# Performance work log

Hardware: AMD Instinct MI355X
Metric: run time of the kernel (lower is better)

The kernel has to match this reference:

```python
import jax, jax.numpy as jnp
import numpy as np

N, D, H, E = 50000, 128, 128, 800000

def _layernorm(h, g, b, eps=1e-5):
    m = jnp.mean(h, axis=-1, keepdims=True)
    v = jnp.mean((h - m) ** 2, axis=-1, keepdims=True)
    return (h - m) * jax.lax.rsqrt(v + eps) * g + b

def setup_inputs() -> dict:
    key = jax.random.key(0)
    ks = jax.random.split(key, 24)
    s = 0.02
    inp = {
        "x": jax.random.normal(ks[0], (N, D), dtype=jnp.float32),
        "edge_index": jax.random.randint(ks[1], (2, E), 0, N, dtype=jnp.int64),
        "degree": jax.random.uniform(ks[2], (N, 1), dtype=jnp.float32) * 32.0,
        "W_lin": jax.random.normal(ks[3], (D, H), jnp.float32) * s,
        "b_lin": jnp.zeros((H,), jnp.float32),
        "Wa1": jax.random.normal(ks[4], (H, H), jnp.float32) * s,
        "ba1": jnp.zeros((H,), jnp.float32),
        "Wa2": jax.random.normal(ks[5], (H, H), jnp.float32) * s,
        "ba2": jnp.zeros((H,), jnp.float32),
        "Wb1": jax.random.normal(ks[6], (H, H), jnp.float32) * s,
        "bb1": jnp.zeros((H,), jnp.float32),
        "Wb2": jax.random.normal(ks[7], (H, H), jnp.float32) * s,
        "bb2": jnp.zeros((H,), jnp.float32),
        "Wg1": jax.random.normal(ks[8], (H, H), jnp.float32) * s,
        "bg1": jnp.zeros((H,), jnp.float32),
        "Wg2": jax.random.normal(ks[9], (H, H), jnp.float32) * s,
        "bg2": jnp.zeros((H,), jnp.float32),
        "Wf1": jax.random.normal(ks[10], (H, H), jnp.float32) * s,
        "bf1": jnp.zeros((H,), jnp.float32),
        "Wf2": jax.random.normal(ks[11], (H, H), jnp.float32) * s,
        "bf2": jnp.zeros((H,), jnp.float32),
        "ln_g": jnp.ones((H,), jnp.float32),
        "ln_b": jnp.zeros((H,), jnp.float32),
    }
    return inp

def reference(x, edge_index, degree, W_lin, b_lin, Wa1, ba1, Wa2, ba2,
              Wb1, bb1, Wb2, bb2, Wg1, bg1, Wg2, bg2, Wf1, bf1, Wf2, bf2,
              ln_g, ln_b):
    # Dropout layers are identity (eval mode)
    h = x @ W_lin + b_lin                                  # [N,H]
    x_res = _layernorm(h, ln_g, ln_b)
    alpha = jax.nn.softplus(jax.nn.relu(h @ Wa1 + ba1) @ Wa2 + ba2)
    beta = jax.nn.softplus(jax.nn.relu(h @ Wb1 + bb1) @ Wb2 + bb2)
    gamma = jax.nn.gelu(h @ Wg1 + bg1, approximate=False) @ Wg2 + bg2
    src, dst = edge_index[0], edge_index[1]
    agg = jax.ops.segment_sum(h[src], dst, num_segments=h.shape[0])  # [N,H]
    y = (beta * agg + gamma) / (alpha + beta * degree)
    z = jax.nn.gelu(y @ Wf1 + bf1, approximate=False) @ Wf2 + bf2
    return z + x_res
```

## Files before the change

kernel.cpp:

```cpp
#include <hip/hip_runtime.h>
#include <hip/hip_bf16.h>
#include <math.h>

#define NODES 50000
#define NEDGE 800000
#define NT_TILES 782
#define NBUCK 98
#define BSHIFT 9
#define BCAP 10240
#define NP1 195
#define EPB1 4104

typedef __bf16 bf16_t;
typedef __bf16 bf16x8 __attribute__((ext_vector_type(8)));
typedef float floatx4 __attribute__((ext_vector_type(4)));

__device__ __forceinline__ float bfbits2f(unsigned int hi16) {
    union { unsigned int u; float f; } c; c.u = hi16; return c.f;
}
__device__ __forceinline__ unsigned short f2bfbits(float f) {
    bf16_t b = (bf16_t)f; unsigned short u;
    __builtin_memcpy(&u, &b, 2); return u;
}

__device__ __forceinline__ float act_rt(float v, int act) {
    if (act == 1) return fmaxf(v, 0.f);
    if (act == 2) {
        float w = 0.79788456f * (v + 0.044715f * v * v * v);
        float e = __expf(2.f * w);
        float th = 1.f - 2.f / (e + 1.f);
        return 0.5f * v * (1.f + th);
    }
    if (act == 3) return fmaxf(v, 0.f) + __logf(1.f + __expf(-fabsf(v)));
    return v;
}

__global__ __launch_bounds__(256) void prep_w_zero(
    const float* __restrict__ w0, const float* __restrict__ w1,
    const float* __restrict__ w2, const float* __restrict__ w3,
    const float* __restrict__ w4, const float* __restrict__ w5,
    const float* __restrict__ w6, const float* __restrict__ w7,
    const float* __restrict__ w8, bf16_t* __restrict__ wt,
    int* __restrict__ gcur)
{
    if (blockIdx.x >= 9) {
        if (threadIdx.x < NBUCK) gcur[threadIdx.x] = 0;
        return;
    }
    const float* Ws[9] = {w0, w1, w2, w3, w4, w5, w6, w7, w8};
    const float* W = Ws[blockIdx.x];
    bf16_t* o = wt + blockIdx.x * 16384;
    for (int idx = threadIdx.x; idx < 16384; idx += 256) {
        int k = idx >> 7, n = idx & 127;
        o[n * 128 + k] = (bf16_t)W[idx];
    }
}

__device__ __forceinline__ void load_w_regs(const bf16_t* __restrict__ W,
                                            uint4 (&wr)[8], int t)
{
    for (int i = 0; i < 8; ++i) {
        int c = t + i * 256;
        int row = c >> 4, g = c & 15;
        wr[i] = *(const uint4*)(W + row * 128 + g * 8);
    }
}
__device__ __forceinline__ void store_w_regs(const uint4 (&wr)[8],
                                             bf16_t* Bs, int t)
{
    for (int i = 0; i < 8; ++i) {
        int c = t + i * 256;
        int row = c >> 4, g = c & 15;
        *(uint4*)&Bs[row * 128 + ((g ^ (row & 15)) * 8)] = wr[i];
    }
}
__device__ __forceinline__ void afrag_gbf16(const bf16_t* __restrict__ A,
        bf16x8 (&af)[4], int r0, int lane, int wave, int M)
{
    int gr = r0 + wave * 16 + (lane & 15);
    gr = min(gr, M - 1);
    const bf16_t* p = A + (size_t)gr * 128 + (lane >> 4) * 8;
    for (int kc = 0; kc < 4; ++kc)
        af[kc] = *(const bf16x8*)(p + kc * 32);
}
__device__ __forceinline__ void kloop64(const bf16x8 (&af)[4], const bf16_t* Bs,
                                        floatx4 (&acc)[8], int l15, int quad)
{
    for (int ni = 0; ni < 8; ++ni)
        for (int r = 0; r < 4; ++r) acc[ni][r] = 0.f;
    for (int kc = 0; kc < 4; ++kc) {
        int kg = kc * 4 + quad;
        bf16x8 b[8];
        for (int ni = 0; ni < 8; ++ni) {
            int row = ni * 16 + l15;
            b[ni] = *(const bf16x8*)&Bs[row * 128 + ((kg ^ l15) * 8)];
        }
        for (int ni = 0; ni < 8; ++ni)
            acc[ni] = __builtin_amdgcn_mfma_f32_16x16x32_bf16(
                af[kc], b[ni], acc[ni], 0, 0, 0);
    }
}
__device__ __forceinline__ void write_Csw(bf16_t* Csw, floatx4 (&acc)[8],
        const float (&bias_r)[8], int lane, int wave, int act)
{
    const int l15 = lane & 15, quad = lane >> 4;
    for (int ni = 0; ni < 8; ++ni) {
        int col = ni * 16 + l15;
        for (int r = 0; r < 4; ++r) {
            int row = wave * 16 + quad * 4 + r;
            float v = act_rt(acc[ni][r] + bias_r[ni], act);
            Csw[row * 128 + (((col >> 3) ^ (row & 15)) << 3) + (col & 7)] = (bf16_t)v;
        }
    }
}
__device__ __forceinline__ void afrag_Csw(const bf16_t* Csw, bf16x8 (&af)[4],
                                          int lane, int wave)
{
    int l15 = lane & 15, quad = lane >> 4;
    int row = wave * 16 + l15;
    for (int kc = 0; kc < 4; ++kc) {
        int kg = kc * 4 + quad;
        af[kc] = *(const bf16x8*)&Csw[row * 128 + ((kg ^ l15) * 8)];
    }
}
__device__ __forceinline__ void copy_Csw_out(const bf16_t* Csw,
        bf16_t* __restrict__ out, int t, int r0, int M)
{
    for (int i = 0; i < 4; ++i) {
        int c = t + i * 256;
        int row = c >> 4, g = c & 15;
        int gr = r0 + row;
        if (gr < M)
            *(uint4*)(out + (size_t)gr * 128 + g * 8) =
                *(const uint4*)&Csw[row * 128 + ((g ^ (row & 15)) * 8)];
    }
}

__global__ __launch_bounds__(256, 3) void hln_p1(
    const float* __restrict__ x, const bf16_t* __restrict__ wt,
    const float* __restrict__ b_lin,
    const float* __restrict__ ln_g, const float* __restrict__ ln_b,
    bf16_t* __restrict__ h, bf16_t* __restrict__ xres,
    const int* __restrict__ ei, int* __restrict__ gcur,
    unsigned* __restrict__ ebuf, int M)
{
    __shared__ __align__(16) char smem[49152];
    const int t = threadIdx.x;
    const int bid = blockIdx.x;

    if (bid % 5 == 4) {
        int* lcnt  = (int*)smem;
        int* lbase = lcnt + NBUCK;
        if (t < NBUCK) lcnt[t] = 0;
        __syncthreads();
        int p1id = bid / 5;
        int base = p1id * EPB1;
        int e_end = min(base + EPB1, NEDGE);
        for (int e = base + t; e < e_end; e += 256)
            atomicAdd(&lcnt[ei[NEDGE + e] >> BSHIFT], 1);
        __syncthreads();
        if (t < NBUCK) {
            lbase[t] = atomicAdd(&gcur[t], lcnt[t]);
            lcnt[t] = 0;
        }
        __syncthreads();
        for (int e = base + t; e < e_end; e += 256) {
            int d = ei[NEDGE + e];
            int s = ei[e];
            int b = d >> BSHIFT;
            int off = atomicAdd(&lcnt[b], 1);
            int pos = lbase[b] + off;
            if (pos < BCAP)
                ebuf[(size_t)b * BCAP + pos] =
                    (unsigned)s | ((unsigned)(d & 511) << 16);
        }
        return;
    }

    bf16_t* Bs  = (bf16_t*)smem;
    bf16_t* Csw = (bf16_t*)(smem + 32768);
    const int tile = bid - bid / 5;
    const int r0 = tile * 64;
    const int lane = t & 63, wave = t >> 6, l15 = lane & 15, quad = lane >> 4;
    uint4 wr[8];
    bf16x8 af[4];
    floatx4 acc[8];
    float bias_r[8];
    for (int ni = 0; ni < 8; ++ni) bias_r[ni] = b_lin[ni * 16 + l15];

    {
        int gr = min(r0 + wave * 16 + l15, M - 1);
        const float* p = x + (size_t)gr * 128 + quad * 8;
        for (int kc = 0; kc < 4; ++kc) {
            float4 u0 = *(const float4*)(p + kc * 32);
            float4 u1 = *(const float4*)(p + kc * 32 + 4);
            bf16x8 f;
            f[0] = (bf16_t)u0.x; f[1] = (bf16_t)u0.y;
            f[2] = (bf16_t)u0.z; f[3] = (bf16_t)u0.w;
            f[4] = (bf16_t)u1.x; f[5] = (bf16_t)u1.y;
            f[6] = (bf16_t)u1.z; f[7] = (bf16_t)u1.w;
            af[kc] = f;
        }
    }
    load_w_regs(wt, wr, t);
    store_w_regs(wr, Bs, t);
    __syncthreads();
    kloop64(af, Bs, acc, l15, quad);
    write_Csw(Csw, acc, bias_r, lane, wave, 0);
    __syncthreads();

    int row = t >> 2, p4 = t & 3;
    int gr = r0 + row;
    uint4 raw[4];
    float vals[32];
    float s = 0.f, sq = 0.f;
    for (int i = 0; i < 4; ++i) {
        int lg = p4 * 4 + i;
        raw[i] = *(const uint4*)&Csw[row * 128 + ((lg ^ (row & 15)) * 8)];
        const unsigned* u = (const unsigned*)&raw[i];
        for (int k = 0; k < 4; ++k) {
            float f0 = bfbits2f(u[k] << 16);
            float f1 = bfbits2f(u[k] & 0xffff0000u);
            vals[i * 8 + k * 2] = f0; vals[i * 8 + k * 2 + 1] = f1;
            s += f0 + f1; sq += f0 * f0 + f1 * f1;
        }
    }
    s += __shfl_xor(s, 1, 64);  sq += __shfl_xor(sq, 1, 64);
    s += __shfl_xor(s, 2, 64);  sq += __shfl_xor(sq, 2, 64);
    float m   = s * (1.f / 128.f);
    float var = fmaxf(sq * (1.f / 128.f) - m * m, 0.f);
    float rs  = rsqrtf(var + 1e-5f);
    if (gr < M) {
        for (int i = 0; i < 4; ++i) {
            int lg = p4 * 4 + i;
            *(uint4*)(h + (size_t)gr * 128 + lg * 8) = raw[i];
            unsigned short ob[8];
            for (int k = 0; k < 8; ++k) {
                int col = lg * 8 + k;
                ob[k] = f2bfbits((vals[i * 8 + k] - m) * rs * ln_g[col] + ln_b[col]);
            }
            uint4 o;
            o.x = ob[0] | ((unsigned)ob[1] << 16);
            o.y = ob[2] | ((unsigned)ob[3] << 16);
            o.z = ob[4] | ((unsigned)ob[5] << 16);
            o.w = ob[6] | ((unsigned)ob[7] << 16);
            *(uint4*)(xres + (size_t)gr * 128 + lg * 8) = o;
        }
    }
}

__global__ __launch_bounds__(256, 3) void branch_p2(
    const bf16_t* __restrict__ h, const bf16_t* __restrict__ wt,
    const float* __restrict__ ba1, const float* __restrict__ ba2,
    const float* __restrict__ bb1, const float* __restrict__ bb2,
    const float* __restrict__ bg1, const float* __restrict__ bg2,
    bf16_t* __restrict__ al, bf16_t* __restrict__ be, bf16_t* __restrict__ ga,
    const int* __restrict__ gcur, const unsigned* __restrict__ ebuf,
    int* __restrict__ off_start, int* __restrict__ cntN,
    int* __restrict__ srcs, int M)
{
    __shared__ __align__(16) char smem[49152];
    const int t = threadIdx.x;
    const int bid = blockIdx.x;

    if (bid % 25 == 24) {
        int* ncnt = (int*)smem;
        int* sa   = ncnt + 512;
        int* sb   = sa + 512;
        int* ncur = sb + 512;
        int* red  = ncur + 512;
        const int b = bid / 25;
        int total = min(gcur[b], BCAP);

        int v = 0;
        for (int j = t; j < b; j += 256) v += min(gcur[j], BCAP);
        for (int o = 1; o < 64; o <<= 1) v += __shfl_xor(v, o, 64);
        if ((t & 63) == 0) red[t >> 6] = v;
        ncnt[t] = 0; ncnt[t + 256] = 0;
        __syncthreads();
        int bucketBase = red[0] + red[1] + red[2] + red[3];

        const unsigned* eb = ebuf + (size_t)b * BCAP;
        for (int i = t; i < total; i += 256)
            atomicAdd(&ncnt[eb[i] >> 16], 1);
        __syncthreads();
        sa[t] = ncnt[t]; sa[t + 256] = ncnt[t + 256];
        __syncthreads();
        int* pin = sa; int* pout = sb;
        for (int o = 1; o < 512; o <<= 1) {
            for (int j = t; j < 512; j += 256)
                pout[j] = pin[j] + (j >= o ? pin[j - o] : 0);
            __syncthreads();
            int* tmp = pin; pin = pout; pout = tmp;
        }
        for (int j = t; j < 512; j += 256) {
            int excl = pin[j] - ncnt[j];
            int node = (b << BSHIFT) + j;
            if (node < NODES) {
                off_start[node] = bucketBase + excl;
                cntN[node] = ncnt[j];
            }
            ncur[j] = excl;
        }
        __syncthreads();
        for (int i = t; i < total; i += 256) {
            unsigned p = eb[i];
            int dl = p >> 16;
            int pos = atomicAdd(&ncur[dl], 1);
            srcs[bucketBase + pos] = (int)(p & 0xFFFFu);
        }
        return;
    }

    const int tile = bid - bid / 25;
    if (tile >= 3 * NT_TILES) return;
    bf16_t* Bs  = (bf16_t*)smem;
    bf16_t* Csw = (bf16_t*)(smem + 32768);
    const int branch = tile / NT_TILES;
    const int r0 = (tile % NT_TILES) * 64;
    const int lane = t & 63, wave = t >> 6, l15 = lane & 15, quad = lane >> 4;
    uint4 wr[8];
    bf16x8 af[4];
    floatx4 acc[8];

    const bf16_t* w1 = wt + (1 + 2 * branch) * 16384;
    const bf16_t* w2 = wt + (2 + 2 * branch) * 16384;
    const float* b1p = (branch == 0) ? ba1 : (branch == 1) ? bb1 : bg1;
    const float* b2p = (branch == 0) ? ba2 : (branch == 1) ? bb2 : bg2;
    bf16_t* out = (branch == 0) ? al : (branch == 1) ? be : ga;
    const int act1 = (branch == 2) ? 2 : 1;
    const int act2 = (branch == 2) ? 0 : 3;

    float b1_r[8], b2_r[8];
    for (int ni = 0; ni < 8; ++ni) {
        b1_r[ni] = b1p[ni * 16 + l15];
        b2_r[ni] = b2p[ni * 16 + l15];
    }

    afrag_gbf16(h, af, r0, lane, wave, M);
    load_w_regs(w1, wr, t);
    store_w_regs(wr, Bs, t);
    load_w_regs(w2, wr, t);
    __syncthreads();

    kloop64(af, Bs, acc, l15, quad);
    write_Csw(Csw, acc, b1_r, lane, wave, act1);
    __syncthreads();
    store_w_regs(wr, Bs, t);
    __syncthreads();

    afrag_Csw(Csw, af, lane, wave);
    kloop64(af, Bs, acc, l15, quad);
    __syncthreads();
    write_Csw(Csw, acc, b2_r, lane, wave, act2);
    __syncthreads();
    copy_Csw_out(Csw, out, t, r0, M);
}

__global__ __launch_bounds__(256, 3) void fused_out(
    const bf16_t* __restrict__ y, const bf16_t* __restrict__ wt,
    const float* __restrict__ bf1, const float* __restrict__ bf2,
    const bf16_t* __restrict__ xres, float* __restrict__ out, int M)
{
    __shared__ __align__(16) char smem[49152];
    bf16_t* Bs  = (bf16_t*)smem;
    bf16_t* Csw = (bf16_t*)(smem + 32768);
    float*  Cf  = (float*)smem;
    const int t = threadIdx.x;
    const int r0 = blockIdx.x * 64;
    const int lane = t & 63, wave = t >> 6, l15 = lane & 15, quad = lane >> 4;
    uint4 wr[8];
    bf16x8 af[4];
    floatx4 acc[8];

    float b1_r[8], b2_r[8];
    for (int ni = 0; ni < 8; ++ni) {
        b1_r[ni] = bf1[ni * 16 + l15];
        b2_r[ni] = bf2[ni * 16 + l15];
    }

    afrag_gbf16(y, af, r0, lane, wave, M);
    load_w_regs(wt + 7 * 16384, wr, t);
    store_w_regs(wr, Bs, t);
    load_w_regs(wt + 8 * 16384, wr, t);
    __syncthreads();

    kloop64(af, Bs, acc, l15, quad);
    write_Csw(Csw, acc, b1_r, lane, wave, 2);
    __syncthreads();
    store_w_regs(wr, Bs, t);
    __syncthreads();

    afrag_Csw(Csw, af, lane, wave);
    kloop64(af, Bs, acc, l15, quad);
    __syncthreads();

    for (int ni = 0; ni < 8; ++ni) {
        int col = ni * 16 + l15;
        for (int r = 0; r < 4; ++r) {
            int row = wave * 16 + quad * 4 + r;
            Cf[row * 132 + col] = acc[ni][r] + b2_r[ni];
        }
    }
    __syncthreads();
    for (int i = 0; i < 8; ++i) {
        int c = t + i * 256;
        int row = c >> 5, q = c & 31;
        int gr = r0 + row;
        if (gr < M) {
            float4 v = *(const float4*)&Cf[row * 132 + q * 4];
            uint2 xr = *(const uint2*)(xres + (size_t)gr * 128 + q * 4);
            v.x += bfbits2f(xr.x << 16);
            v.y += bfbits2f(xr.x & 0xffff0000u);
            v.z += bfbits2f(xr.y << 16);
            v.w += bfbits2f(xr.y & 0xffff0000u);
            *(float4*)(out + (size_t)gr * 128 + q * 4) = v;
        }
    }
}

__global__ __launch_bounds__(256) void gather_y_kernel(
    const int* __restrict__ off_start, const int* __restrict__ cnt,
    const int* __restrict__ srcs, const bf16_t* __restrict__ h,
    const bf16_t* __restrict__ al, const bf16_t* __restrict__ be,
    const bf16_t* __restrict__ ga, const float* __restrict__ deg,
    bf16_t* __restrict__ y, int M)
{
    int wave = threadIdx.x >> 6, lane = threadIdx.x & 63;
    int node = blockIdx.x * 4 + wave;
    if (node >= M) return;
    int s0 = __builtin_amdgcn_readfirstlane(off_start[node]);
    int n  = __builtin_amdgcn_readfirstlane(cnt[node]);
    int grp = lane >> 4, c16 = lane & 15;
    float a[8] = {0.f, 0.f, 0.f, 0.f, 0.f, 0.f, 0.f, 0.f};

    for (int j = 0; j < n; j += 8) {
        int e0 = j + grp, e1 = j + 4 + grp;
        int i0 = srcs[s0 + min(e0, n - 1)];
        int i1 = srcs[s0 + min(e1, n - 1)];
        uint4 v0 = *(const uint4*)(h + (size_t)i0 * 128 + c16 * 8);
        uint4 v1 = *(const uint4*)(h + (size_t)i1 * 128 + c16 * 8);
        if (e0 < n) {
            const unsigned* u = (const unsigned*)&v0;
            for (int k = 0; k < 4; ++k) {
                a[2 * k]     += bfbits2f(u[k] << 16);
                a[2 * k + 1] += bfbits2f(u[k] & 0xffff0000u);
            }
        }
        if (e1 < n) {
            const unsigned* u = (const unsigned*)&v1;
            for (int k = 0; k < 4; ++k) {
                a[2 * k]     += bfbits2f(u[k] << 16);
                a[2 * k + 1] += bfbits2f(u[k] & 0xffff0000u);
            }
        }
    }
    for (int k = 0; k < 8; ++k) {
        a[k] += __shfl_xor(a[k], 16, 64);
        a[k] += __shfl_xor(a[k], 32, 64);
    }
    if (lane < 16) {
        size_t i0 = (size_t)node * 128 + (size_t)c16 * 8;
        uint4 ra = *(const uint4*)(al + i0);
        uint4 rb = *(const uint4*)(be + i0);
        uint4 rg = *(const uint4*)(ga + i0);
        float d = deg[node];
        const unsigned* ua = (const unsigned*)&ra;
        const unsigned* ub = (const unsigned*)&rb;
        const unsigned* ug = (const unsigned*)&rg;
        unsigned short o[8];
        for (int k = 0; k < 4; ++k) {
            float a0 = bfbits2f(ua[k] << 16), a1 = bfbits2f(ua[k] & 0xffff0000u);
            float b0 = bfbits2f(ub[k] << 16), b1 = bfbits2f(ub[k] & 0xffff0000u);
            float g0 = bfbits2f(ug[k] << 16), g1 = bfbits2f(ug[k] & 0xffff0000u);
            o[2 * k]     = f2bfbits((b0 * a[2 * k]     + g0) / (a0 + b0 * d));
            o[2 * k + 1] = f2bfbits((b1 * a[2 * k + 1] + g1) / (a1 + b1 * d));
        }
        uint4 ov;
        ov.x = o[0] | ((unsigned)o[1] << 16);
        ov.y = o[2] | ((unsigned)o[3] << 16);
        ov.z = o[4] | ((unsigned)o[5] << 16);
        ov.w = o[6] | ((unsigned)o[7] << 16);
        *(uint4*)(y + i0) = ov;
    }
}

extern "C" void kernel_launch(void* const* d_in, const int* in_sizes, int n_in,
                              void* d_out, int out_size, void* d_ws, size_t ws_size,
                              hipStream_t stream)
{
    const float* x    = (const float*)d_in[0];
    const int*   ei   = (const int*)d_in[1];
    const float* deg  = (const float*)d_in[2];
    const float* W_lin = (const float*)d_in[3];  const float* b_lin = (const float*)d_in[4];
    const float* Wa1 = (const float*)d_in[5];    const float* ba1 = (const float*)d_in[6];
    const float* Wa2 = (const float*)d_in[7];    const float* ba2 = (const float*)d_in[8];
    const float* Wb1 = (const float*)d_in[9];    const float* bb1 = (const float*)d_in[10];
    const float* Wb2 = (const float*)d_in[11];   const float* bb2 = (const float*)d_in[12];
    const float* Wg1 = (const float*)d_in[13];   const float* bg1 = (const float*)d_in[14];
    const float* Wg2 = (const float*)d_in[15];   const float* bg2 = (const float*)d_in[16];
    const float* Wf1 = (const float*)d_in[17];   const float* bf1 = (const float*)d_in[18];
    const float* Wf2 = (const float*)d_in[19];   const float* bf2 = (const float*)d_in[20];
    const float* ln_g = (const float*)d_in[21];  const float* ln_b = (const float*)d_in[22];

    const int M = NODES;
    const size_t NB2 = (size_t)M * 128 * 2;

    char* ws = (char*)d_ws;
    size_t off = 0;
    bf16_t* wt  = (bf16_t*)(ws + off); off += (size_t)9 * 16384 * 2;
    bf16_t* h   = (bf16_t*)(ws + off); off += NB2;
    bf16_t* al  = (bf16_t*)(ws + off); off += NB2;
    bf16_t* be  = (bf16_t*)(ws + off); off += NB2;
    bf16_t* ga  = (bf16_t*)(ws + off); off += NB2;
    bf16_t* yv  = (bf16_t*)(ws + off); off += NB2;
    bf16_t* xres = (bf16_t*)(ws + off); off += NB2;
    int* gcur      = (int*)(ws + off); off += 128 * 4;
    int* off_start = (int*)(ws + off); off += (size_t)NODES * 4 + 64;
    int* cntN      = (int*)(ws + off); off += (size_t)NODES * 4 + 64;
    int* srcs      = (int*)(ws + off); off += (size_t)NEDGE * 4;
    unsigned* ebuf = (unsigned*)(ws + off); off += (size_t)NBUCK * BCAP * 4;
    float* outp = (float*)d_out;

    dim3 blk(256);

    prep_w_zero<<<10, blk, 0, stream>>>(
        W_lin, Wa1, Wa2, Wb1, Wb2, Wg1, Wg2, Wf1, Wf2, wt, gcur);

    hln_p1<<<977, blk, 0, stream>>>(
        x, wt, b_lin, ln_g, ln_b, h, xres, ei, gcur, ebuf, M);

    branch_p2<<<2450, blk, 0, stream>>>(
        h, wt, ba1, ba2, bb1, bb2, bg1, bg2, al, be, ga,
        gcur, ebuf, off_start, cntN, srcs, M);

    gather_y_kernel<<<(M + 3) / 4, blk, 0, stream>>>(off_start, cntN, srcs, h,
                                                     al, be, ga, deg, yv, M);
    fused_out<<<NT_TILES, blk, 0, stream>>>(yv, wt, bf1, bf2, xres, outp, M);
}
```

Measured before the change: 278.5 us.

## Replace CSR build and gather with LDS-atomic bucket aggregation and fuse branches into one kernel

The per-node CSR construction in branch_p2 and the separate gather_y kernel are removed. Edges are now bucketed into 128-node buckets (391 buckets), and a new gather_agg kernel accumulates h rows into a 64KB shared-memory fp32 accumulator with LDS atomics, writing agg as bf16. The alpha, beta and gamma MLP branches, the y combination and the final MLP are fused into one 'mega' kernel per 64-row tile, so the al/be/ga/y intermediates no longer go through HBM. In exchange, gather_agg runs only 391 blocks with heavy LDS atomic contention, the mega kernel holds more registers at 2 blocks per CU, and each bucket is capped at 2560 edges, which could silently drop edges on skewed graphs.

```diff
diff --git a/kernel.cpp b/kernel.cpp
--- a/kernel.cpp
+++ b/kernel.cpp
@@ -5,9 +5,9 @@
 #define NODES 50000
 #define NEDGE 800000
 #define NT_TILES 782
-#define NBUCK 98
-#define BSHIFT 9
-#define BCAP 10240
+#define NBUCK 391
+#define BSHIFT 7
+#define BCAP 2560
 #define NP1 195
 #define EPB1 4104
 
@@ -44,7 +44,7 @@
     int* __restrict__ gcur)
 {
     if (blockIdx.x >= 9) {
-        if (threadIdx.x < NBUCK) gcur[threadIdx.x] = 0;
+        for (int j = threadIdx.x; j < NBUCK; j += 256) gcur[j] = 0;
         return;
     }
     const float* Ws[9] = {w0, w1, w2, w3, w4, w5, w6, w7, w8};
@@ -123,18 +123,6 @@
         af[kc] = *(const bf16x8*)&Csw[row * 128 + ((kg ^ l15) * 8)];
     }
 }
-__device__ __forceinline__ void copy_Csw_out(const bf16_t* Csw,
-        bf16_t* __restrict__ out, int t, int r0, int M)
-{
-    for (int i = 0; i < 4; ++i) {
-        int c = t + i * 256;
-        int row = c >> 4, g = c & 15;
-        int gr = r0 + row;
-        if (gr < M)
-            *(uint4*)(out + (size_t)gr * 128 + g * 8) =
-                *(const uint4*)&Csw[row * 128 + ((g ^ (row & 15)) * 8)];
-    }
-}
 
 __global__ __launch_bounds__(256, 3) void hln_p1(
     const float* __restrict__ x, const bf16_t* __restrict__ wt,
@@ -151,7 +139,7 @@
     if (bid % 5 == 4) {
         int* lcnt  = (int*)smem;
         int* lbase = lcnt + NBUCK;
-        if (t < NBUCK) lcnt[t] = 0;
+        for (int j = t; j < NBUCK; j += 256) lcnt[j] = 0;
         __syncthreads();
         int p1id = bid / 5;
         int base = p1id * EPB1;
@@ -159,9 +147,9 @@
         for (int e = base + t; e < e_end; e += 256)
             atomicAdd(&lcnt[ei[NEDGE + e] >> BSHIFT], 1);
         __syncthreads();
-        if (t < NBUCK) {
-            lbase[t] = atomicAdd(&gcur[t], lcnt[t]);
-            lcnt[t] = 0;
+        for (int j = t; j < NBUCK; j += 256) {
+            lbase[j] = atomicAdd(&gcur[j], lcnt[j]);
+            lcnt[j] = 0;
         }
         __syncthreads();
         for (int e = base + t; e < e_end; e += 256) {
@@ -172,7 +160,7 @@
             int pos = lbase[b] + off;
             if (pos < BCAP)
                 ebuf[(size_t)b * BCAP + pos] =
-                    (unsigned)s | ((unsigned)(d & 511) << 16);
+                    (unsigned)s | ((unsigned)(d & 127) << 16);
         }
         return;
     }
@@ -249,117 +237,109 @@
     }
 }
 
-__global__ __launch_bounds__(256, 3) void branch_p2(
+__global__ __launch_bounds__(512, 4) void gather_agg(
+    const int* __restrict__ gcur, const unsigned* __restrict__ ebuf,
+    const bf16_t* __restrict__ h, bf16_t* __restrict__ agg, int M)
+{
+    __shared__ float acc[16384];
+    const int t = threadIdx.x;
+    {
+        float4 z; z.x = 0.f; z.y = 0.f; z.z = 0.f; z.w = 0.f;
+        for (int i = t; i < 4096; i += 512) *(float4*)&acc[i * 4] = z;
+    }
+    __syncthreads();
+    const int b = blockIdx.x;
+    const int total = min(gcur[b], BCAP);
+    const unsigned* eb = ebuf + (size_t)b * BCAP;
+    const int wave = t >> 6, lane = t & 63;
+    const int half = lane >> 5, l31 = lane & 31;
+    const unsigned short* hu = (const unsigned short*)h;
+
+    unsigned pkc[4];
+    const int base0 = wave * 8;
+    #pragma unroll
+    for (int k = 0; k < 4; ++k)
+        pkc[k] = (total > 0) ? eb[min(base0 + 2 * k + half, total - 1)] : 0u;
+
+    for (int base = base0; base < total; base += 64) {
+        unsigned pk[4];
+        #pragma unroll
+        for (int k = 0; k < 4; ++k) pk[k] = pkc[k];
+        ushort4 hr[4];
+        #pragma unroll
+        for (int k = 0; k < 4; ++k)
+            hr[k] = *(const ushort4*)(hu + (size_t)(pk[k] & 0xFFFFu) * 128 + l31 * 4);
+        int nb = base + 64;
+        if (nb < total) {
+            #pragma unroll
+            for (int k = 0; k < 4; ++k)
+                pkc[k] = eb[min(nb + 2 * k + half, total - 1)];
+        }
+        #pragma unroll
+        for (int k = 0; k < 4; ++k) {
+            if (base + 2 * k + half < total) {
+                float* ap = acc + ((pk[k] >> 16) & 127) * 128 + l31;
+                atomicAdd(ap,      bfbits2f((unsigned)hr[k].x << 16));
+                atomicAdd(ap + 32, bfbits2f((unsigned)hr[k].y << 16));
+                atomicAdd(ap + 64, bfbits2f((unsigned)hr[k].z << 16));
+                atomicAdd(ap + 96, bfbits2f((unsigned)hr[k].w << 16));
+            }
+        }
+    }
+    __syncthreads();
+    const int node0 = b << BSHIFT;
+    for (int i = t; i < 2048; i += 512) {
+        int row = i >> 4, g = i & 15;
+        int gr = node0 + row;
+        if (gr < M) {
+            unsigned short ob[8];
+            #pragma unroll
+            for (int k = 0; k < 8; ++k) {
+                int c = g * 8 + k;
+                ob[k] = f2bfbits(acc[row * 128 + ((c & 3) << 5) + (c >> 2)]);
+            }
+            uint4 o;
+            o.x = ob[0] | ((unsigned)ob[1] << 16);
+            o.y = ob[2] | ((unsigned)ob[3] << 16);
+            o.z = ob[4] | ((unsigned)ob[5] << 16);
+            o.w = ob[6] | ((unsigned)ob[7] << 16);
+            *(uint4*)(agg + (size_t)gr * 128 + g * 8) = o;
+        }
+    }
+}
+
+__device__ __forceinline__ void two_layer(
+    const bf16_t* __restrict__ wt, int w2i, int wni,
+    const float* __restrict__ B1, const float* __restrict__ B2, int act1,
+    const bf16x8 (&af_h)[4], bf16x8 (&af_t)[4],
+    uint4 (&wr)[8], floatx4 (&acc)[8],
+    float (&b1_r)[8], float (&b2_r)[8],
+    bf16_t* Bs, bf16_t* Csw, int t, int lane, int wave, int l15, int quad)
+{
+    store_w_regs(wr, Bs, t);
+    for (int ni = 0; ni < 8; ++ni) {
+        b1_r[ni] = B1[ni * 16 + l15];
+        b2_r[ni] = B2[ni * 16 + l15];
+    }
+    __syncthreads();
+    kloop64(af_h, Bs, acc, l15, quad);
+    load_w_regs(wt + w2i * 16384, wr, t);
+    write_Csw(Csw, acc, b1_r, lane, wave, act1);
+    __syncthreads();
+    store_w_regs(wr, Bs, t);
+    afrag_Csw(Csw, af_t, lane, wave);
+    load_w_regs(wt + wni * 16384, wr, t);
+    __syncthreads();
+    kloop64(af_t, Bs, acc, l15, quad);
+}
+
+__global__ __launch_bounds__(256, 2) void mega(
     const bf16_t* __restrict__ h, const bf16_t* __restrict__ wt,
     const float* __restrict__ ba1, const float* __restrict__ ba2,
     const float* __restrict__ bb1, const float* __restrict__ bb2,
     const float* __restrict__ bg1, const float* __restrict__ bg2,
-    bf16_t* __restrict__ al, bf16_t* __restrict__ be, bf16_t* __restrict__ ga,
-    const int* __restrict__ gcur, const unsigned* __restrict__ ebuf,
-    int* __restrict__ off_start, int* __restrict__ cntN,
-    int* __restrict__ srcs, int M)
-{
-    __shared__ __align__(16) char smem[49152];
-    const int t = threadIdx.x;
-    const int bid = blockIdx.x;
-
-    if (bid % 25 == 24) {
-        int* ncnt = (int*)smem;
-        int* sa   = ncnt + 512;
-        int* sb   = sa + 512;
-        int* ncur = sb + 512;
-        int* red  = ncur + 512;
-        const int b = bid / 25;
-        int total = min(gcur[b], BCAP);
-
-        int v = 0;
-        for (int j = t; j < b; j += 256) v += min(gcur[j], BCAP);
-        for (int o = 1; o < 64; o <<= 1) v += __shfl_xor(v, o, 64);
-        if ((t & 63) == 0) red[t >> 6] = v;
-        ncnt[t] = 0; ncnt[t + 256] = 0;
-        __syncthreads();
-        int bucketBase = red[0] + red[1] + red[2] + red[3];
-
-        const unsigned* eb = ebuf + (size_t)b * BCAP;
-        for (int i = t; i < total; i += 256)
-            atomicAdd(&ncnt[eb[i] >> 16], 1);
-        __syncthreads();
-        sa[t] = ncnt[t]; sa[t + 256] = ncnt[t + 256];
-        __syncthreads();
-        int* pin = sa; int* pout = sb;
-        for (int o = 1; o < 512; o <<= 1) {
-            for (int j = t; j < 512; j += 256)
-                pout[j] = pin[j] + (j >= o ? pin[j - o] : 0);
-            __syncthreads();
-            int* tmp = pin; pin = pout; pout = tmp;
-        }
-        for (int j = t; j < 512; j += 256) {
-            int excl = pin[j] - ncnt[j];
-            int node = (b << BSHIFT) + j;
-            if (node < NODES) {
-                off_start[node] = bucketBase + excl;
-                cntN[node] = ncnt[j];
-            }
-            ncur[j] = excl;
-        }
-        __syncthreads();
-        for (int i = t; i < total; i += 256) {
-            unsigned p = eb[i];
-            int dl = p >> 16;
-            int pos = atomicAdd(&ncur[dl], 1);
-            srcs[bucketBase + pos] = (int)(p & 0xFFFFu);
-        }
-        return;
-    }
-
-    const int tile = bid - bid / 25;
-    if (tile >= 3 * NT_TILES) return;
-    bf16_t* Bs  = (bf16_t*)smem;
-    bf16_t* Csw = (bf16_t*)(smem + 32768);
-    const int branch = tile / NT_TILES;
-    const int r0 = (tile % NT_TILES) * 64;
-    const int lane = t & 63, wave = t >> 6, l15 = lane & 15, quad = lane >> 4;
-    uint4 wr[8];
-    bf16x8 af[4];
-    floatx4 acc[8];
-
-    const bf16_t* w1 = wt + (1 + 2 * branch) * 16384;
-    const bf16_t* w2 = wt + (2 + 2 * branch) * 16384;
-    const float* b1p = (branch == 0) ? ba1 : (branch == 1) ? bb1 : bg1;
-    const float* b2p = (branch == 0) ? ba2 : (branch == 1) ? bb2 : bg2;
-    bf16_t* out = (branch == 0) ? al : (branch == 1) ? be : ga;
-    const int act1 = (branch == 2) ? 2 : 1;
-    const int act2 = (branch == 2) ? 0 : 3;
-
-    float b1_r[8], b2_r[8];
-    for (int ni = 0; ni < 8; ++ni) {
-        b1_r[ni] = b1p[ni * 16 + l15];
-        b2_r[ni] = b2p[ni * 16 + l15];
-    }
-
-    afrag_gbf16(h, af, r0, lane, wave, M);
-    load_w_regs(w1, wr, t);
-    store_w_regs(wr, Bs, t);
-    load_w_regs(w2, wr, t);
-    __syncthreads();
-
-    kloop64(af, Bs, acc, l15, quad);
-    write_Csw(Csw, acc, b1_r, lane, wave, act1);
-    __syncthreads();
-    store_w_regs(wr, Bs, t);
-    __syncthreads();
-
-    afrag_Csw(Csw, af, lane, wave);
-    kloop64(af, Bs, acc, l15, quad);
-    __syncthreads();
-    write_Csw(Csw, acc, b2_r, lane, wave, act2);
-    __syncthreads();
-    copy_Csw_out(Csw, out, t, r0, M);
-}
-
-__global__ __launch_bounds__(256, 3) void fused_out(
-    const bf16_t* __restrict__ y, const bf16_t* __restrict__ wt,
     const float* __restrict__ bf1, const float* __restrict__ bf2,
+    const bf16_t* __restrict__ agg, const float* __restrict__ deg,
     const bf16_t* __restrict__ xres, float* __restrict__ out, int M)
 {
     __shared__ __align__(16) char smem[49152];
@@ -370,36 +350,89 @@
     const int r0 = blockIdx.x * 64;
     const int lane = t & 63, wave = t >> 6, l15 = lane & 15, quad = lane >> 4;
     uint4 wr[8];
-    bf16x8 af[4];
+    bf16x8 af_h[4], af_t[4];
     floatx4 acc[8];
-
     float b1_r[8], b2_r[8];
+    float al_r[8][4], be_r[8][4];
+
+    afrag_gbf16(h, af_h, r0, lane, wave, M);
+    load_w_regs(wt + 1 * 16384, wr, t);
+
+    two_layer(wt, 2, 3, ba1, ba2, 1, af_h, af_t, wr, acc, b1_r, b2_r,
+              Bs, Csw, t, lane, wave, l15, quad);
+    #pragma unroll
+    for (int ni = 0; ni < 8; ++ni)
+        #pragma unroll
+        for (int r = 0; r < 4; ++r)
+            al_r[ni][r] = act_rt(acc[ni][r] + b2_r[ni], 3);
+    __syncthreads();
+
+    two_layer(wt, 4, 5, bb1, bb2, 1, af_h, af_t, wr, acc, b1_r, b2_r,
+              Bs, Csw, t, lane, wave, l15, quad);
+    #pragma unroll
+    for (int ni = 0; ni < 8; ++ni)
+        #pragma unroll
+        for (int r = 0; r < 4; ++r)
+            be_r[ni][r] = act_rt(acc[ni][r] + b2_r[ni], 3);
+    __syncthreads();
+
+    two_layer(wt, 6, 7, bg1, bg2, 2, af_h, af_t, wr, acc, b1_r, b2_r,
+              Bs, Csw, t, lane, wave, l15, quad);
+
+    for (int i = 0; i < 4; ++i) {
+        int c = t + i * 256;
+        int row = c >> 4, g = c & 15;
+        int gr = min(r0 + row, M - 1);
+        *(uint4*)&Csw[row * 128 + g * 8] = *(const uint4*)(agg + (size_t)gr * 128 + g * 8);
+    }
+    float dg_r[4];
+    #pragma unroll
+    for (int r = 0; r < 4; ++r)
+        dg_r[r] = deg[min(r0 + wave * 16 + quad * 4 + r, M - 1)];
+    __syncthreads();
+
+    #pragma unroll
+    for (int ni = 0; ni < 8; ++ni) {
+        int col = ni * 16 + l15;
+        #pragma unroll
+        for (int r = 0; r < 4; ++r) {
+            int row = wave * 16 + quad * 4 + r;
+            float aggv = (float)Csw[row * 128 + col];
+            float ga = acc[ni][r] + b2_r[ni];
+            float alv = al_r[ni][r], bev = be_r[ni][r];
+            acc[ni][r] = (bev * aggv + ga) / (alv + bev * dg_r[r]);
+        }
+    }
+    __syncthreads();
+
+    store_w_regs(wr, Bs, t);
+    {
+        float zb[8] = {0.f, 0.f, 0.f, 0.f, 0.f, 0.f, 0.f, 0.f};
+        write_Csw(Csw, acc, zb, lane, wave, 0);
+    }
+    load_w_regs(wt + 8 * 16384, wr, t);
     for (int ni = 0; ni < 8; ++ni) {
         b1_r[ni] = bf1[ni * 16 + l15];
         b2_r[ni] = bf2[ni * 16 + l15];
     }
-
-    afrag_gbf16(y, af, r0, lane, wave, M);
-    load_w_regs(wt + 7 * 16384, wr, t);
+    __syncthreads();
+    afrag_Csw(Csw, af_t, lane, wave);
+    kloop64(af_t, Bs, acc, l15, quad);
+    __syncthreads();
+    write_Csw(Csw, acc, b1_r, lane, wave, 2);
     store_w_regs(wr, Bs, t);
-    load_w_regs(wt + 8 * 16384, wr, t);
-    __syncthreads();
-
-    kloop64(af, Bs, acc, l15, quad);
-    write_Csw(Csw, acc, b1_r, lane, wave, 2);
-    __syncthreads();
-    store_w_regs(wr, Bs, t);
-    __syncthreads();
-
-    afrag_Csw(Csw, af, lane, wave);
-    kloop64(af, Bs, acc, l15, quad);
-    __syncthreads();
-
+    __syncthreads();
+    afrag_Csw(Csw, af_t, lane, wave);
+    kloop64(af_t, Bs, acc, l15, quad);
+    __syncthreads();
+
+    #pragma unroll
     for (int ni = 0; ni < 8; ++ni) {
         int col = ni * 16 + l15;
+        #pragma unroll
         for (int r = 0; r < 4; ++r) {
             int row = wave * 16 + quad * 4 + r;
-            Cf[row * 132 + col] = acc[ni][r] + b2_r[ni];
+            Cf[row * 128 + col] = acc[ni][r] + b2_r[ni];
         }
     }
     __syncthreads();
@@ -408,7 +441,7 @@
         int row = c >> 5, q = c & 31;
         int gr = r0 + row;
         if (gr < M) {
-            float4 v = *(const float4*)&Cf[row * 132 + q * 4];
+            float4 v = *(const float4*)&Cf[row * 128 + q * 4];
             uint2 xr = *(const uint2*)(xres + (size_t)gr * 128 + q * 4);
             v.x += bfbits2f(xr.x << 16);
             v.y += bfbits2f(xr.x & 0xffff0000u);
@@ -416,72 +449,6 @@
             v.w += bfbits2f(xr.y & 0xffff0000u);
             *(float4*)(out + (size_t)gr * 128 + q * 4) = v;
         }
-    }
-}
-
-__global__ __launch_bounds__(256) void gather_y_kernel(
-    const int* __restrict__ off_start, const int* __restrict__ cnt,
-    const int* __restrict__ srcs, const bf16_t* __restrict__ h,
-    const bf16_t* __restrict__ al, const bf16_t* __restrict__ be,
-    const bf16_t* __restrict__ ga, const float* __restrict__ deg,
-    bf16_t* __restrict__ y, int M)
-{
-    int wave = threadIdx.x >> 6, lane = threadIdx.x & 63;
-    int node = blockIdx.x * 4 + wave;
-    if (node >= M) return;
-    int s0 = __builtin_amdgcn_readfirstlane(off_start[node]);
-    int n  = __builtin_amdgcn_readfirstlane(cnt[node]);
-    int grp = lane >> 4, c16 = lane & 15;
-    float a[8] = {0.f, 0.f, 0.f, 0.f, 0.f, 0.f, 0.f, 0.f};
-
-    for (int j = 0; j < n; j += 8) {
-        int e0 = j + grp, e1 = j + 4 + grp;
-        int i0 = srcs[s0 + min(e0, n - 1)];
-        int i1 = srcs[s0 + min(e1, n - 1)];
-        uint4 v0 = *(const uint4*)(h + (size_t)i0 * 128 + c16 * 8);
-        uint4 v1 = *(const uint4*)(h + (size_t)i1 * 128 + c16 * 8);
-        if (e0 < n) {
-            const unsigned* u = (const unsigned*)&v0;
-            for (int k = 0; k < 4; ++k) {
-                a[2 * k]     += bfbits2f(u[k] << 16);
-                a[2 * k + 1] += bfbits2f(u[k] & 0xffff0000u);
-            }
-        }
-        if (e1 < n) {
-            const unsigned* u = (const unsigned*)&v1;
-            for (int k = 0; k < 4; ++k) {
-                a[2 * k]     += bfbits2f(u[k] << 16);
-                a[2 * k + 1] += bfbits2f(u[k] & 0xffff0000u);
-            }
-        }
-    }
-    for (int k = 0; k < 8; ++k) {
-        a[k] += __shfl_xor(a[k], 16, 64);
-        a[k] += __shfl_xor(a[k], 32, 64);
-    }
-    if (lane < 16) {
-        size_t i0 = (size_t)node * 128 + (size_t)c16 * 8;
-        uint4 ra = *(const uint4*)(al + i0);
-        uint4 rb = *(const uint4*)(be + i0);
-        uint4 rg = *(const uint4*)(ga + i0);
-        float d = deg[node];
-        const unsigned* ua = (const unsigned*)&ra;
-        const unsigned* ub = (const unsigned*)&rb;
-        const unsigned* ug = (const unsigned*)&rg;
-        unsigned short o[8];
-        for (int k = 0; k < 4; ++k) {
-            float a0 = bfbits2f(ua[k] << 16), a1 = bfbits2f(ua[k] & 0xffff0000u);
-            float b0 = bfbits2f(ub[k] << 16), b1 = bfbits2f(ub[k] & 0xffff0000u);
-            float g0 = bfbits2f(ug[k] << 16), g1 = bfbits2f(ug[k] & 0xffff0000u);
-            o[2 * k]     = f2bfbits((b0 * a[2 * k]     + g0) / (a0 + b0 * d));
-            o[2 * k + 1] = f2bfbits((b1 * a[2 * k + 1] + g1) / (a1 + b1 * d));
-        }
-        uint4 ov;
-        ov.x = o[0] | ((unsigned)o[1] << 16);
-        ov.y = o[2] | ((unsigned)o[3] << 16);
-        ov.z = o[4] | ((unsigned)o[5] << 16);
-        ov.w = o[6] | ((unsigned)o[7] << 16);
-        *(uint4*)(y + i0) = ov;
     }
 }
 
@@ -508,17 +475,11 @@
 
     char* ws = (char*)d_ws;
     size_t off = 0;
-    bf16_t* wt  = (bf16_t*)(ws + off); off += (size_t)9 * 16384 * 2;
-    bf16_t* h   = (bf16_t*)(ws + off); off += NB2;
-    bf16_t* al  = (bf16_t*)(ws + off); off += NB2;
-    bf16_t* be  = (bf16_t*)(ws + off); off += NB2;
-    bf16_t* ga  = (bf16_t*)(ws + off); off += NB2;
-    bf16_t* yv  = (bf16_t*)(ws + off); off += NB2;
+    bf16_t* wt   = (bf16_t*)(ws + off); off += (size_t)9 * 16384 * 2;
+    bf16_t* h    = (bf16_t*)(ws + off); off += NB2;
     bf16_t* xres = (bf16_t*)(ws + off); off += NB2;
-    int* gcur      = (int*)(ws + off); off += 128 * 4;
-    int* off_start = (int*)(ws + off); off += (size_t)NODES * 4 + 64;
-    int* cntN      = (int*)(ws + off); off += (size_t)NODES * 4 + 64;
-    int* srcs      = (int*)(ws + off); off += (size_t)NEDGE * 4;
+    bf16_t* agg  = (bf16_t*)(ws + off); off += NB2;
+    int* gcur      = (int*)(ws + off); off += 512 * 4;
     unsigned* ebuf = (unsigned*)(ws + off); off += (size_t)NBUCK * BCAP * 4;
     float* outp = (float*)d_out;
 
@@ -527,14 +488,12 @@
     prep_w_zero<<<10, blk, 0, stream>>>(
         W_lin, Wa1, Wa2, Wb1, Wb2, Wg1, Wg2, Wf1, Wf2, wt, gcur);
 
-    hln_p1<<<977, blk, 0, stream>>>(
+    hln_p1<<<NT_TILES + NP1, blk, 0, stream>>>(
         x, wt, b_lin, ln_g, ln_b, h, xres, ei, gcur, ebuf, M);
 
-    branch_p2<<<2450, blk, 0, stream>>>(
-        h, wt, ba1, ba2, bb1, bb2, bg1, bg2, al, be, ga,
-        gcur, ebuf, off_start, cntN, srcs, M);
-
-    gather_y_kernel<<<(M + 3) / 4, blk, 0, stream>>>(off_start, cntN, srcs, h,
-                                                     al, be, ga, deg, yv, M);
-    fused_out<<<NT_TILES, blk, 0, stream>>>(yv, wt, bf1, bf2, xres, outp, M);
-}
+    gather_agg<<<NBUCK, dim3(512), 0, stream>>>(gcur, ebuf, h, agg, M);
+
+    mega<<<NT_TILES, blk, 0, stream>>>(
+        h, wt, ba1, ba2, bb1, bb2, bg1, bg2, bf1, bf2,
+        agg, deg, xres, outp, M);
+}
```

Result: slower. 944.3 us (+239.0%).

## Merge three branch MLPs per tile and deepen gather loads

Applied to the files above, without the earlier changes.

Each block in the branch kernel now runs all three branch MLPs (alpha, beta, gamma) on one 64-row tile. The h fragment is loaded once instead of three times, and the next weight matrix is prefetched into registers while the current one is used. The grid drops from 2450 to 891 blocks, and the bucket-sort blocks are now interleaved every 9th block instead of every 25th. Separately, the gather loop issues four independent row loads per iteration instead of two to expose more memory-level parallelism. The costs are fewer blocks, which means less parallelism, and higher register pressure from holding two fragment sets.

```diff
diff --git a/kernel.cpp b/kernel.cpp
--- a/kernel.cpp
+++ b/kernel.cpp
@@ -249,7 +249,7 @@
     }
 }
 
-__global__ __launch_bounds__(256, 3) void branch_p2(
+__global__ __launch_bounds__(256, 3) void branch_all(
     const bf16_t* __restrict__ h, const bf16_t* __restrict__ wt,
     const float* __restrict__ ba1, const float* __restrict__ ba2,
     const float* __restrict__ bb1, const float* __restrict__ bb2,
@@ -263,13 +263,14 @@
     const int t = threadIdx.x;
     const int bid = blockIdx.x;
 
-    if (bid % 25 == 24) {
+    if (bid % 9 == 8) {
         int* ncnt = (int*)smem;
         int* sa   = ncnt + 512;
         int* sb   = sa + 512;
         int* ncur = sb + 512;
         int* red  = ncur + 512;
-        const int b = bid / 25;
+        const int b = bid / 9;
+        if (b >= NBUCK) return;
         int total = min(gcur[b], BCAP);
 
         int v = 0;
@@ -312,110 +313,48 @@
         return;
     }
 
-    const int tile = bid - bid / 25;
-    if (tile >= 3 * NT_TILES) return;
+    const int tile = bid - bid / 9;
+    if (tile >= NT_TILES) return;
     bf16_t* Bs  = (bf16_t*)smem;
     bf16_t* Csw = (bf16_t*)(smem + 32768);
-    const int branch = tile / NT_TILES;
-    const int r0 = (tile % NT_TILES) * 64;
+    const int r0 = tile * 64;
     const int lane = t & 63, wave = t >> 6, l15 = lane & 15, quad = lane >> 4;
     uint4 wr[8];
-    bf16x8 af[4];
+    bf16x8 af_h[4], af_t[4];
     floatx4 acc[8];
-
-    const bf16_t* w1 = wt + (1 + 2 * branch) * 16384;
-    const bf16_t* w2 = wt + (2 + 2 * branch) * 16384;
-    const float* b1p = (branch == 0) ? ba1 : (branch == 1) ? bb1 : bg1;
-    const float* b2p = (branch == 0) ? ba2 : (branch == 1) ? bb2 : bg2;
-    bf16_t* out = (branch == 0) ? al : (branch == 1) ? be : ga;
-    const int act1 = (branch == 2) ? 2 : 1;
-    const int act2 = (branch == 2) ? 0 : 3;
-
     float b1_r[8], b2_r[8];
-    for (int ni = 0; ni < 8; ++ni) {
-        b1_r[ni] = b1p[ni * 16 + l15];
-        b2_r[ni] = b2p[ni * 16 + l15];
-    }
-
-    afrag_gbf16(h, af, r0, lane, wave, M);
-    load_w_regs(w1, wr, t);
-    store_w_regs(wr, Bs, t);
-    load_w_regs(w2, wr, t);
-    __syncthreads();
-
-    kloop64(af, Bs, acc, l15, quad);
-    write_Csw(Csw, acc, b1_r, lane, wave, act1);
-    __syncthreads();
-    store_w_regs(wr, Bs, t);
-    __syncthreads();
-
-    afrag_Csw(Csw, af, lane, wave);
-    kloop64(af, Bs, acc, l15, quad);
-    __syncthreads();
-    write_Csw(Csw, acc, b2_r, lane, wave, act2);
-    __syncthreads();
-    copy_Csw_out(Csw, out, t, r0, M);
-}
-
-__global__ __launch_bounds__(256, 3) void fused_out(
-    const bf16_t* __restrict__ y, const bf16_t* __restrict__ wt,
-    const float* __restrict__ bf1, const float* __restrict__ bf2,
-    const bf16_t* __restrict__ xres, float* __restrict__ out, int M)
-{
-    __shared__ __align__(16) char smem[49152];
-    bf16_t* Bs  = (bf16_t*)smem;
-    bf16_t* Csw = (bf16_t*)(smem + 32768);
-    float*  Cf  = (float*)smem;
-    const int t = threadIdx.x;
-    const int r0 = blockIdx.x * 64;
-    const int lane = t & 63, wave = t >> 6, l15 = lane & 15, quad = lane >> 4;
-    uint4 wr[8];
-    bf16x8 af[4];
-    floatx4 acc[8];
-
-    float b1_r[8], b2_r[8];
-    for (int ni = 0; ni < 8; ++ni) {
-        b1_r[ni] = bf1[ni * 16 + l15];
-        b2_r[ni] = bf2[ni * 16 + l15];
-    }
-
-    afrag_gbf16(y, af, r0, lane, wave, M);
-    load_w_regs(wt + 7 * 16384, wr, t);
-    store_w_regs(wr, Bs, t);
-    load_w_regs(wt + 8 * 16384, wr, t);
-    __syncthreads();
-
-    kloop64(af, Bs, acc, l15, quad);
-    write_Csw(Csw, acc, b1_r, lane, wave, 2);
-    __syncthreads();
-    store_w_regs(wr, Bs, t);
-    __syncthreads();
-
-    afrag_Csw(Csw, af, lane, wave);
-    kloop64(af, Bs, acc, l15, quad);
-    __syncthreads();
-
-    for (int ni = 0; ni < 8; ++ni) {
-        int col = ni * 16 + l15;
-        for (int r = 0; r < 4; ++r) {
-            int row = wave * 16 + quad * 4 + r;
-            Cf[row * 132 + col] = acc[ni][r] + b2_r[ni];
-        }
-    }
-    __syncthreads();
-    for (int i = 0; i < 8; ++i) {
-        int c = t + i * 256;
-        int row = c >> 5, q = c & 31;
-        int gr = r0 + row;
-        if (gr < M) {
-            float4 v = *(const float4*)&Cf[row * 132 + q * 4];
-            uint2 xr = *(const uint2*)(xres + (size_t)gr * 128 + q * 4);
-            v.x += bfbits2f(xr.x << 16);
-            v.y += bfbits2f(xr.x & 0xffff0000u);
-            v.z += bfbits2f(xr.y << 16);
-            v.w += bfbits2f(xr.y & 0xffff0000u);
-            *(float4*)(out + (size_t)gr * 128 + q * 4) = v;
-        }
+
+    const float* B1s[3] = {ba1, bb1, bg1};
+    const float* B2s[3] = {ba2, bb2, bg2};
+    bf16_t* outs[3] = {al, be, ga};
+    const int act1s[3] = {1, 1, 2};
+    const int act2s[3] = {3, 3, 0};
+
+    afrag_gbf16(h, af_h, r0, lane, wave, M);
+    load_w_regs(wt + 1 * 16384, wr, t);
+
+    #pragma unroll
+    for (int b = 0; b < 3; ++b) {
+        store_w_regs(wr, Bs, t);
+        load_w_regs(wt + (2 + 2 * b) * 16384, wr, t);
+        for (int ni = 0; ni < 8; ++ni) {
+            b1_r[ni] = B1s[b][ni * 16 + l15];
+            b2_r[ni] = B2s[b][ni * 16 + l15];
+        }
+        __syncthreads();
+        kloop64(af_h, Bs, acc, l15, quad);
+        write_Csw(Csw, acc, b1_r, lane, wave, act1s[b]);
+        __syncthreads();
+        store_w_regs(wr, Bs, t);
+        afrag_Csw(Csw, af_t, lane, wave);
+        if (b < 2)
+            load_w_regs(wt + (3 + 2 * b) * 16384, wr, t);
+        __syncthreads();
+        kloop64(af_t, Bs, acc, l15, quad);
+        __syncthreads();
+        write_Csw(Csw, acc, b2_r, lane, wave, act2s[b]);
+        __syncthreads();
+        copy_Csw_out(Csw, outs[b], t, r0, M);
     }
 }
 
@@ -434,24 +373,24 @@
     int grp = lane >> 4, c16 = lane & 15;
     float a[8] = {0.f, 0.f, 0.f, 0.f, 0.f, 0.f, 0.f, 0.f};
 
-    for (int j = 0; j < n; j += 8) {
-        int e0 = j + grp, e1 = j + 4 + grp;
-        int i0 = srcs[s0 + min(e0, n - 1)];
-        int i1 = srcs[s0 + min(e1, n - 1)];
-        uint4 v0 = *(const uint4*)(h + (size_t)i0 * 128 + c16 * 8);
-        uint4 v1 = *(const uint4*)(h + (size_t)i1 * 128 + c16 * 8);
-        if (e0 < n) {
-            const unsigned* u = (const unsigned*)&v0;
-            for (int k = 0; k < 4; ++k) {
-                a[2 * k]     += bfbits2f(u[k] << 16);
-                a[2 * k + 1] += bfbits2f(u[k] & 0xffff0000u);
-            }
-        }
-        if (e1 < n) {
-            const unsigned* u = (const unsigned*)&v1;
-            for (int k = 0; k < 4; ++k) {
-                a[2 * k]     += bfbits2f(u[k] << 16);
-                a[2 * k + 1] += bfbits2f(u[k] & 0xffff0000u);
+    for (int j = 0; j < n; j += 16) {
+        int idx[4];
+        #pragma unroll
+        for (int s = 0; s < 4; ++s)
+            idx[s] = srcs[s0 + min(j + 4 * s + grp, n - 1)];
+        uint4 v[4];
+        #pragma unroll
+        for (int s = 0; s < 4; ++s)
+            v[s] = *(const uint4*)(h + (size_t)idx[s] * 128 + c16 * 8);
+        #pragma unroll
+        for (int s = 0; s < 4; ++s) {
+            if (j + 4 * s + grp < n) {
+                const unsigned* u = (const unsigned*)&v[s];
+                #pragma unroll
+                for (int k = 0; k < 4; ++k) {
+                    a[2 * k]     += bfbits2f(u[k] << 16);
+                    a[2 * k + 1] += bfbits2f(u[k] & 0xffff0000u);
+                }
             }
         }
     }
@@ -485,6 +424,68 @@
     }
 }
 
+__global__ __launch_bounds__(256, 3) void fused_out(
+    const bf16_t* __restrict__ y, const bf16_t* __restrict__ wt,
+    const float* __restrict__ bf1, const float* __restrict__ bf2,
+    const bf16_t* __restrict__ xres, float* __restrict__ out, int M)
+{
+    __shared__ __align__(16) char smem[49152];
+    bf16_t* Bs  = (bf16_t*)smem;
+    bf16_t* Csw = (bf16_t*)(smem + 32768);
+    float*  Cf  = (float*)smem;
+    const int t = threadIdx.x;
+    const int r0 = blockIdx.x * 64;
+    const int lane = t & 63, wave = t >> 6, l15 = lane & 15, quad = lane >> 4;
+    uint4 wr[8];
+    bf16x8 af[4];
+    floatx4 acc[8];
+
+    float b1_r[8], b2_r[8];
+    for (int ni = 0; ni < 8; ++ni) {
+        b1_r[ni] = bf1[ni * 16 + l15];
+        b2_r[ni] = bf2[ni * 16 + l15];
+    }
+
+    afrag_gbf16(y, af, r0, lane, wave, M);
+    load_w_regs(wt + 7 * 16384, wr, t);
+    store_w_regs(wr, Bs, t);
+    load_w_regs(wt + 8 * 16384, wr, t);
+    __syncthreads();
+
+    kloop64(af, Bs, acc, l15, quad);
+    write_Csw(Csw, acc, b1_r, lane, wave, 2);
+    __syncthreads();
+    store_w_regs(wr, Bs, t);
+    __syncthreads();
+
+    afrag_Csw(Csw, af, lane, wave);
+    kloop64(af, Bs, acc, l15, quad);
+    __syncthreads();
+
+    for (int ni = 0; ni < 8; ++ni) {
+        int col = ni * 16 + l15;
+        for (int r = 0; r < 4; ++r) {
+            int row = wave * 16 + quad * 4 + r;
+            Cf[row * 132 + col] = acc[ni][r] + b2_r[ni];
+        }
+    }
+    __syncthreads();
+    for (int i = 0; i < 8; ++i) {
+        int c = t + i * 256;
+        int row = c >> 5, q = c & 31;
+        int gr = r0 + row;
+        if (gr < M) {
+            float4 v = *(const float4*)&Cf[row * 132 + q * 4];
+            uint2 xr = *(const uint2*)(xres + (size_t)gr * 128 + q * 4);
+            v.x += bfbits2f(xr.x << 16);
+            v.y += bfbits2f(xr.x & 0xffff0000u);
+            v.z += bfbits2f(xr.y << 16);
+            v.w += bfbits2f(xr.y & 0xffff0000u);
+            *(float4*)(out + (size_t)gr * 128 + q * 4) = v;
+        }
+    }
+}
+
 extern "C" void kernel_launch(void* const* d_in, const int* in_sizes, int n_in,
                               void* d_out, int out_size, void* d_ws, size_t ws_size,
                               hipStream_t stream)
@@ -530,7 +531,7 @@
     hln_p1<<<977, blk, 0, stream>>>(
         x, wt, b_lin, ln_g, ln_b, h, xres, ei, gcur, ebuf, M);
 
-    branch_p2<<<2450, blk, 0, stream>>>(
+    branch_all<<<891, blk, 0, stream>>>(
         h, wt, ba1, ba2, bb1, bb2, bg1, bg2, al, be, ga,
         gcur, ebuf, off_start, cntN, srcs, M);
 
```

After: 289.5 us. +4.0%, slower.
